# Kernel optimization log

Measured on AMD Instinct MI355X. Metric: run time of the kernel, lower is better.

The kernel has to match this reference:

```python
import jax, jax.numpy as jnp
import numpy as np
from math import log2, ceil

NUM_LEAVES = 128
KERNEL = 8
STRIDE = 8
PADDING = 0
LR = 0.3

LEAF_NUM = 2 ** ceil(log2(NUM_LEAVES))   # 128
DEPTH = int(log2(LEAF_NUM))              # 7
NUM_NODES = 2 * LEAF_NUM - 1             # 255


def _ancestor_table():
    # A[j-1, t-1] = global heap index of the ancestor of node j at tree level t,
    # or -1 if t exceeds j's own level. Nodes use heap indexing: children of i
    # are 2i+1, 2i+2 (matches the layer bookkeeping in the torch module).
    A = np.full((NUM_NODES - 1, DEPTH), -1, dtype=np.int32)
    for j in range(1, NUM_NODES):
        lvl = int(np.floor(np.log2(j + 1)))
        anc = j
        for t in range(lvl, 0, -1):
            A[j - 1, t - 1] = anc
            anc = (anc - 1) // 2
    return jnp.asarray(A)

_ANC = _ancestor_table()  # (NUM_NODES-1, DEPTH)


def img2patches(x):
    x = jnp.pad(x, PADDING)
    H, W = x.shape
    n0 = (H - KERNEL) // STRIDE + 1
    n1 = (W - KERNEL) // STRIDE + 1
    win = jnp.arange(KERNEL)
    rows = jnp.arange(n0)[:, None] * STRIDE + win[None, :]  # (n0, k)
    cols = jnp.arange(n1)[:, None] * STRIDE + win[None, :]  # (n1, k)
    p = x[rows[:, None, :, None], cols[None, :, None, :]]   # (n0, n1, k, k)
    return p.reshape(n0 * n1, KERNEL * KERNEL)


def setup_inputs() -> dict:
    key = jax.random.key(0)
    k1, k2 = jax.random.split(key)
    image = jax.random.uniform(k1, (2048, 2048), dtype=jnp.float32)
    nodes = jax.random.uniform(k2, (NUM_NODES, KERNEL * KERNEL), dtype=jnp.float32)
    return {"image": image, "nodes": nodes}


def reference(image, nodes):
    X = img2patches(image)                      # (P, k^2)
    P = X.shape[0]

    # --- hierarchical BMU descent (binary tree, DEPTH levels) ---
    cur = jnp.zeros((P,), dtype=jnp.int32)      # root
    bmu_levels = []
    for _ in range(DEPTH):
        c0 = 2 * cur + 1
        c1 = 2 * cur + 2
        # pnorm with p=2 in the source is (sum((a-b)^2))^2 -- monotone, kept faithful
        d0 = jnp.sum((nodes[c0] - X) ** 2, axis=-1) ** 2
        d1 = jnp.sum((nodes[c1] - X) ** 2, axis=-1) ** 2
        cur = jnp.where(d1 < d0, c1, c0)        # tie -> first (c0), like torch.min
        bmu_levels.append(cur)
    bmu_path = jnp.stack(bmu_levels, axis=1)    # (P, DEPTH), bmu at levels 1..DEPTH

    # --- layer_state for every non-root node: number of levels at which the
    # node's ancestor coincides with the BMU chain (== the torch concatenated
    # layer_state, columns ordered by global node index 1..NUM_NODES-1) ---
    state = jnp.sum(_ANC[None, :, :] == bmu_path[:, None, :], axis=-1)  # (P, N-1)

    lrates = LR * (2.0 ** jnp.arange(1, DEPTH + 2, dtype=jnp.float32)) / 2.0 ** (DEPTH + 1)
    lrs = lrates[state]                          # (P, N-1)

    # mean_p lrs[p,j] * (X[p,:] - nodes[1+j,:])
    #   = (lrs^T @ X)/P - mean_p(lrs)[:,None] * nodes[1:]
    upd = jnp.einsum('pj,pk->jk', lrs, X) / P - lrs.mean(axis=0)[:, None] * nodes[1:]
    new_nodes = nodes.at[1:].add(upd)

    return new_nodes, cur[:, None]               # updated codebook, leaf BMU per patch
```

## Files before the change

kernel.cpp:

```cpp
#include <hip/hip_runtime.h>

#define IMG_W 2048
#define NUM_NODES 255
#define NLEAF 128
#define DEPTH 7
#define RS 68

template<int CTRL>
__device__ __forceinline__ float dpp_add(float x) {
    int v = __builtin_amdgcn_update_dpp(0, __float_as_int(x), CTRL, 0xF, 0xF, true);
    return x + __int_as_float(v);
}
__device__ __forceinline__ float group16_sum(float x) {
    x = dpp_add<0xB1>(x);
    x = dpp_add<0x4E>(x);
    x = dpp_add<0x141>(x);
    x = dpp_add<0x128>(x);
    return x;
}

__global__ __launch_bounds__(1024, 4) void fusedK(const float* __restrict__ img,
                                                  const float* __restrict__ nodes,
                                                  float* __restrict__ leaf_out,
                                                  float* __restrict__ S,
                                                  unsigned* __restrict__ cnt)
{
    __shared__ float nds[NUM_NODES * RS];
    __shared__ float Sl[NLEAF * RS];
    __shared__ unsigned cntl[NLEAF];

    const int t = threadIdx.x;
    const int b = blockIdx.x;
    const int g = t >> 4;
    const int q = t & 15;
    const int q4 = q * 4;

    for (int i = t; i < NLEAF * RS; i += 1024) Sl[i] = 0.0f;
    if (t < NLEAF) cntl[t] = 0u;

    const float4* ng = (const float4*)nodes;
    for (int i = t; i < NUM_NODES * 16; i += 1024) {
        *(float4*)&nds[(i >> 4) * RS + (i & 15) * 4] = ng[i];
    }

    float4 xv0, xv1, xv2, xv3;
    {
        const int roff = (q >> 1), coff = (q & 1) * 4;
        int p = b * 256 + g;
        xv0 = *(const float4*)(img + (size_t)((p >> 8) * 8 + roff) * IMG_W + (p & 255) * 8 + coff);
        p += 64;
        xv1 = *(const float4*)(img + (size_t)((p >> 8) * 8 + roff) * IMG_W + (p & 255) * 8 + coff);
        p += 64;
        xv2 = *(const float4*)(img + (size_t)((p >> 8) * 8 + roff) * IMG_W + (p & 255) * 8 + coff);
        p += 64;
        xv3 = *(const float4*)(img + (size_t)((p >> 8) * 8 + roff) * IMG_W + (p & 255) * 8 + coff);
    }
    __syncthreads();

    int cur0 = 0, cur1 = 0, cur2 = 0, cur3 = 0;
    #pragma unroll
    for (int lvl = 0; lvl < DEPTH; ++lvl) {
        const int ca = 2 * cur0 + 1;
        const int cb = 2 * cur1 + 1;
        const int cc = 2 * cur2 + 1;
        const int cd = 2 * cur3 + 1;
        const float* pa = &nds[ca * RS + q4];
        const float* pb = &nds[cb * RS + q4];
        const float* pc = &nds[cc * RS + q4];
        const float* pd = &nds[cd * RS + q4];
        const float4 A0 = *(const float4*)(pa);
        const float4 B0 = *(const float4*)(pa + RS);
        const float4 A1 = *(const float4*)(pb);
        const float4 B1 = *(const float4*)(pb + RS);
        const float4 A2 = *(const float4*)(pc);
        const float4 B2 = *(const float4*)(pc + RS);
        const float4 A3 = *(const float4*)(pd);
        const float4 B3 = *(const float4*)(pd + RS);

        float d, s0, s1;
        s0 = 0.f; s1 = 0.f;
        d = A0.x - xv0.x; s0 = fmaf(d, d, s0);  d = B0.x - xv0.x; s1 = fmaf(d, d, s1);
        d = A0.y - xv0.y; s0 = fmaf(d, d, s0);  d = B0.y - xv0.y; s1 = fmaf(d, d, s1);
        d = A0.z - xv0.z; s0 = fmaf(d, d, s0);  d = B0.z - xv0.z; s1 = fmaf(d, d, s1);
        d = A0.w - xv0.w; s0 = fmaf(d, d, s0);  d = B0.w - xv0.w; s1 = fmaf(d, d, s1);
        cur0 = (group16_sum(s1 - s0) < 0.0f) ? (ca + 1) : ca;
        s0 = 0.f; s1 = 0.f;
        d = A1.x - xv1.x; s0 = fmaf(d, d, s0);  d = B1.x - xv1.x; s1 = fmaf(d, d, s1);
        d = A1.y - xv1.y; s0 = fmaf(d, d, s0);  d = B1.y - xv1.y; s1 = fmaf(d, d, s1);
        d = A1.z - xv1.z; s0 = fmaf(d, d, s0);  d = B1.z - xv1.z; s1 = fmaf(d, d, s1);
        d = A1.w - xv1.w; s0 = fmaf(d, d, s0);  d = B1.w - xv1.w; s1 = fmaf(d, d, s1);
        cur1 = (group16_sum(s1 - s0) < 0.0f) ? (cb + 1) : cb;
        s0 = 0.f; s1 = 0.f;
        d = A2.x - xv2.x; s0 = fmaf(d, d, s0);  d = B2.x - xv2.x; s1 = fmaf(d, d, s1);
        d = A2.y - xv2.y; s0 = fmaf(d, d, s0);  d = B2.y - xv2.y; s1 = fmaf(d, d, s1);
        d = A2.z - xv2.z; s0 = fmaf(d, d, s0);  d = B2.z - xv2.z; s1 = fmaf(d, d, s1);
        d = A2.w - xv2.w; s0 = fmaf(d, d, s0);  d = B2.w - xv2.w; s1 = fmaf(d, d, s1);
        cur2 = (group16_sum(s1 - s0) < 0.0f) ? (cc + 1) : cc;
        s0 = 0.f; s1 = 0.f;
        d = A3.x - xv3.x; s0 = fmaf(d, d, s0);  d = B3.x - xv3.x; s1 = fmaf(d, d, s1);
        d = A3.y - xv3.y; s0 = fmaf(d, d, s0);  d = B3.y - xv3.y; s1 = fmaf(d, d, s1);
        d = A3.z - xv3.z; s0 = fmaf(d, d, s0);  d = B3.z - xv3.z; s1 = fmaf(d, d, s1);
        d = A3.w - xv3.w; s0 = fmaf(d, d, s0);  d = B3.w - xv3.w; s1 = fmaf(d, d, s1);
        cur3 = (group16_sum(s1 - s0) < 0.0f) ? (cd + 1) : cd;
    }

    if (q == 0) {
        leaf_out[b * 256 + g]       = (float)cur0;
        leaf_out[b * 256 + 64 + g]  = (float)cur1;
        leaf_out[b * 256 + 128 + g] = (float)cur2;
        leaf_out[b * 256 + 192 + g] = (float)cur3;
        atomicAdd(&cntl[cur0 - 127], 1u);
        atomicAdd(&cntl[cur1 - 127], 1u);
        atomicAdd(&cntl[cur2 - 127], 1u);
        atomicAdd(&cntl[cur3 - 127], 1u);
    }

    {
        float* dst = &Sl[(cur0 - 127) * RS + q4];
        atomicAdd(dst + 0, xv0.x); atomicAdd(dst + 1, xv0.y);
        atomicAdd(dst + 2, xv0.z); atomicAdd(dst + 3, xv0.w);
        dst = &Sl[(cur1 - 127) * RS + q4];
        atomicAdd(dst + 0, xv1.x); atomicAdd(dst + 1, xv1.y);
        atomicAdd(dst + 2, xv1.z); atomicAdd(dst + 3, xv1.w);
        dst = &Sl[(cur2 - 127) * RS + q4];
        atomicAdd(dst + 0, xv2.x); atomicAdd(dst + 1, xv2.y);
        atomicAdd(dst + 2, xv2.z); atomicAdd(dst + 3, xv2.w);
        dst = &Sl[(cur3 - 127) * RS + q4];
        atomicAdd(dst + 0, xv3.x); atomicAdd(dst + 1, xv3.y);
        atomicAdd(dst + 2, xv3.z); atomicAdd(dst + 3, xv3.w);
    }
    __syncthreads();

    for (int i = t; i < NLEAF * 64; i += 1024) {
        const float v = Sl[(i >> 6) * RS + (i & 63)];
        if (v != 0.0f) atomicAdd(&S[i], v);
    }
    if (t < NLEAF && cntl[t] != 0u) atomicAdd(&cnt[t], cntl[t]);
}

__global__ __launch_bounds__(256) void updateK(const float* __restrict__ nodes,
                                               const float* __restrict__ S,
                                               const unsigned* __restrict__ cnt,
                                               float* __restrict__ out)
{
    const int gid = blockIdx.x * 256 + threadIdx.x;
    if (gid >= NUM_NODES * 64) return;
    const int n = gid >> 6, k = gid & 63;
    const float nd = nodes[gid];
    if (n == 0) { out[gid] = nd; return; }

    const int pos = n + 1;
    const int Ln = 31 - __clz(pos);
    float su = 0.f, sc = 0.f;
    #pragma unroll 8
    for (int L = 0; L < NLEAF; ++L) {
        const int a = (128 + L) >> (7 - Ln);
        const int x = pos ^ a;
        const int state = (x == 0) ? Ln : (Ln - (31 - __clz(x)) - 1);
        const float lr = 0.3f * ((float)(1 << state) * (1.0f / 128.0f));
        su = fmaf(lr, S[L * 64 + k], su);
        sc = fmaf(lr, (float)cnt[L], sc);
    }
    const float invP = 1.0f / 65536.0f;
    out[gid] = nd + su * invP - (sc * invP) * nd;
}

extern "C" void kernel_launch(void* const* d_in, const int* in_sizes, int n_in,
                              void* d_out, int out_size, void* d_ws, size_t ws_size,
                              hipStream_t stream)
{
    const float* img   = (const float*)d_in[0];
    const float* nodes = (const float*)d_in[1];

    float* out_nodes = (float*)d_out;
    float* out_leaf  = out_nodes + NUM_NODES * 64;

    float*    S   = (float*)d_ws;
    unsigned* cnt = (unsigned*)(S + NLEAF * 64);

    hipMemsetAsync(d_ws, 0, (NLEAF * 64) * sizeof(float) + NLEAF * sizeof(unsigned), stream);
    fusedK<<<256, 1024, 0, stream>>>(img, nodes, out_leaf, S, cnt);
    updateK<<<64, 256, 0, stream>>>(nodes, S, cnt, out_nodes);
}
```

Before: 107.6 us.

## Fuse node update into main kernel via grid-wide completion counter

Drops the separate update kernel launch. Each block bumps a global done-counter, and the first 16 blocks spin until all blocks finish, then compute the codebook update from S and cnt staged in shared memory. The shared-memory accumulation layout is also changed to stride-16 so the per-lane atomics spread across banks, and each block starts its global flush at a different offset to reduce atomic contention. The spin-wait assumes all 256 blocks are co-resident, which holds on this GPU, and it removes one kernel launch gap.

```diff
diff --git a/kernel.cpp b/kernel.cpp
--- a/kernel.cpp
+++ b/kernel.cpp
@@ -5,6 +5,8 @@
 #define NLEAF 128
 #define DEPTH 7
 #define RS 68
+#define NBLK 256
+#define NUPD 16
 
 template<int CTRL>
 __device__ __forceinline__ float dpp_add(float x) {
@@ -23,7 +25,9 @@
                                                   const float* __restrict__ nodes,
                                                   float* __restrict__ leaf_out,
                                                   float* __restrict__ S,
-                                                  unsigned* __restrict__ cnt)
+                                                  unsigned* __restrict__ cnt,
+                                                  unsigned* __restrict__ fdone,
+                                                  float* __restrict__ out_nodes)
 {
     __shared__ float nds[NUM_NODES * RS];
     __shared__ float Sl[NLEAF * RS];
@@ -116,53 +120,73 @@
     }
 
     {
-        float* dst = &Sl[(cur0 - 127) * RS + q4];
-        atomicAdd(dst + 0, xv0.x); atomicAdd(dst + 1, xv0.y);
-        atomicAdd(dst + 2, xv0.z); atomicAdd(dst + 3, xv0.w);
-        dst = &Sl[(cur1 - 127) * RS + q4];
-        atomicAdd(dst + 0, xv1.x); atomicAdd(dst + 1, xv1.y);
-        atomicAdd(dst + 2, xv1.z); atomicAdd(dst + 3, xv1.w);
-        dst = &Sl[(cur2 - 127) * RS + q4];
-        atomicAdd(dst + 0, xv2.x); atomicAdd(dst + 1, xv2.y);
-        atomicAdd(dst + 2, xv2.z); atomicAdd(dst + 3, xv2.w);
-        dst = &Sl[(cur3 - 127) * RS + q4];
-        atomicAdd(dst + 0, xv3.x); atomicAdd(dst + 1, xv3.y);
-        atomicAdd(dst + 2, xv3.z); atomicAdd(dst + 3, xv3.w);
-    }
-    __syncthreads();
-
-    for (int i = t; i < NLEAF * 64; i += 1024) {
-        const float v = Sl[(i >> 6) * RS + (i & 63)];
+        float* base = &Sl[(cur0 - 127) * RS + q];
+        atomicAdd(base +  0, xv0.x); atomicAdd(base + 16, xv0.y);
+        atomicAdd(base + 32, xv0.z); atomicAdd(base + 48, xv0.w);
+        base = &Sl[(cur1 - 127) * RS + q];
+        atomicAdd(base +  0, xv1.x); atomicAdd(base + 16, xv1.y);
+        atomicAdd(base + 32, xv1.z); atomicAdd(base + 48, xv1.w);
+        base = &Sl[(cur2 - 127) * RS + q];
+        atomicAdd(base +  0, xv2.x); atomicAdd(base + 16, xv2.y);
+        atomicAdd(base + 32, xv2.z); atomicAdd(base + 48, xv2.w);
+        base = &Sl[(cur3 - 127) * RS + q];
+        atomicAdd(base +  0, xv3.x); atomicAdd(base + 16, xv3.y);
+        atomicAdd(base + 32, xv3.z); atomicAdd(base + 48, xv3.w);
+    }
+    __syncthreads();
+
+    for (int ii = t; ii < NLEAF * 64; ii += 1024) {
+        const int i = (ii + b * 64) & (NLEAF * 64 - 1);
+        const int e = i & 63;
+        const float v = Sl[(i >> 6) * RS + (e & 3) * 16 + (e >> 2)];
         if (v != 0.0f) atomicAdd(&S[i], v);
     }
     if (t < NLEAF && cntl[t] != 0u) atomicAdd(&cnt[t], cntl[t]);
-}
-
-__global__ __launch_bounds__(256) void updateK(const float* __restrict__ nodes,
-                                               const float* __restrict__ S,
-                                               const unsigned* __restrict__ cnt,
-                                               float* __restrict__ out)
-{
-    const int gid = blockIdx.x * 256 + threadIdx.x;
-    if (gid >= NUM_NODES * 64) return;
-    const int n = gid >> 6, k = gid & 63;
-    const float nd = nodes[gid];
-    if (n == 0) { out[gid] = nd; return; }
-
-    const int pos = n + 1;
-    const int Ln = 31 - __clz(pos);
-    float su = 0.f, sc = 0.f;
-    #pragma unroll 8
-    for (int L = 0; L < NLEAF; ++L) {
-        const int a = (128 + L) >> (7 - Ln);
-        const int x = pos ^ a;
-        const int state = (x == 0) ? Ln : (Ln - (31 - __clz(x)) - 1);
-        const float lr = 0.3f * ((float)(1 << state) * (1.0f / 128.0f));
-        su = fmaf(lr, S[L * 64 + k], su);
-        sc = fmaf(lr, (float)cnt[L], sc);
-    }
-    const float invP = 1.0f / 65536.0f;
-    out[gid] = nd + su * invP - (sc * invP) * nd;
+
+    __syncthreads();
+    if (t == 0) {
+        __threadfence();
+        __hip_atomic_fetch_add(fdone, 1u, __ATOMIC_RELEASE, __HIP_MEMORY_SCOPE_AGENT);
+    }
+    if (b >= NUPD) return;
+
+    if (t == 0) {
+        while (__hip_atomic_load(fdone, __ATOMIC_ACQUIRE, __HIP_MEMORY_SCOPE_AGENT) != NBLK) {}
+    }
+    __syncthreads();
+
+    float* Ss = nds;
+    float* cs = nds + 8192;
+    for (int i = t; i < NLEAF * 64; i += 1024)
+        Ss[i] = __hip_atomic_load(&S[i], __ATOMIC_RELAXED, __HIP_MEMORY_SCOPE_AGENT);
+    if (t < NLEAF)
+        cs[t] = (float)__hip_atomic_load(&cnt[t], __ATOMIC_RELAXED, __HIP_MEMORY_SCOPE_AGENT);
+    __syncthreads();
+
+    const int n = b * 16 + (t >> 6);
+    const int k = t & 63;
+    if (n >= NUM_NODES) return;
+    const float nd = nodes[n * 64 + k];
+    float o;
+    if (n == 0) {
+        o = nd;
+    } else {
+        const int pos = n + 1;
+        const int Ln = 31 - __clz(pos);
+        float su = 0.f, sc = 0.f;
+        #pragma unroll 8
+        for (int L = 0; L < NLEAF; ++L) {
+            const int a = (128 + L) >> (7 - Ln);
+            const int x = pos ^ a;
+            const int state = (x == 0) ? Ln : (Ln - (31 - __clz(x)) - 1);
+            const float lr = 0.3f * ((float)(1 << state) * (1.0f / 128.0f));
+            su = fmaf(lr, Ss[L * 64 + k], su);
+            sc = fmaf(lr, cs[L], sc);
+        }
+        const float invP = 1.0f / 65536.0f;
+        o = nd + su * invP - (sc * invP) * nd;
+    }
+    out_nodes[n * 64 + k] = o;
 }
 
 extern "C" void kernel_launch(void* const* d_in, const int* in_sizes, int n_in,
@@ -175,10 +199,12 @@
     float* out_nodes = (float*)d_out;
     float* out_leaf  = out_nodes + NUM_NODES * 64;
 
-    float*    S   = (float*)d_ws;
-    unsigned* cnt = (unsigned*)(S + NLEAF * 64);
-
-    hipMemsetAsync(d_ws, 0, (NLEAF * 64) * sizeof(float) + NLEAF * sizeof(unsigned), stream);
-    fusedK<<<256, 1024, 0, stream>>>(img, nodes, out_leaf, S, cnt);
-    updateK<<<64, 256, 0, stream>>>(nodes, S, cnt, out_nodes);
-}
+    float*    S     = (float*)d_ws;
+    unsigned* cnt   = (unsigned*)(S + NLEAF * 64);
+    unsigned* fdone = cnt + NLEAF;
+
+    hipMemsetAsync(d_ws, 0,
+                   (NLEAF * 64) * sizeof(float) + NLEAF * sizeof(unsigned) + 16,
+                   stream);
+    fusedK<<<NBLK, 1024, 0, stream>>>(img, nodes, out_leaf, S, cnt, fdone, out_nodes);
+}
```

After: 116.2 us. 8.0% more time.
